# Performance work log

Hardware: AMD Instinct MI355X
Metric: run time of the kernel (lower is better)

Reference implementation:

```python
import jax, jax.numpy as jnp
import numpy as np

N, F_IN, H, C, D, NH, L, FF = 4096, 256, 2, 64, 128, 4, 2, 2048
DEG = 32


def setup_inputs() -> dict:
    key = jax.random.key(0)
    ks = jax.random.split(key, 32)
    s = 0.05
    # graph: random edges + self loops (PyG GATConv adds self loops)
    src = jax.random.randint(ks[0], (N * DEG,), 0, N)
    dst = jax.random.randint(ks[1], (N * DEG,), 0, N)
    loop = jnp.arange(N)
    edge_index = jnp.stack([jnp.concatenate([src, loop]),
                            jnp.concatenate([dst, loop])]).astype(jnp.int64)
    inp = {
        'x': jax.random.normal(ks[2], (N, F_IN), jnp.float32),
        'edge_index': edge_index,
        'enc_w1': jax.random.normal(ks[3], (F_IN, 128), jnp.float32) * s,
        'enc_b1': jnp.zeros((128,), jnp.float32),
        'enc_w2': jax.random.normal(ks[4], (128, D), jnp.float32) * s,
        'enc_b2': jnp.zeros((D,), jnp.float32),
        'gat_w': jax.random.normal(ks[5], (D, H * C), jnp.float32) * s,
        'gat_asrc': jax.random.normal(ks[6], (H, C), jnp.float32) * s,
        'gat_adst': jax.random.normal(ks[7], (H, C), jnp.float32) * s,
        'gat_bias': jnp.zeros((H * C,), jnp.float32),
        't_wq': jax.random.normal(ks[8], (L, D, D), jnp.float32) * s,
        't_bq': jnp.zeros((L, D), jnp.float32),
        't_wk': jax.random.normal(ks[9], (L, D, D), jnp.float32) * s,
        't_bk': jnp.zeros((L, D), jnp.float32),
        't_wv': jax.random.normal(ks[10], (L, D, D), jnp.float32) * s,
        't_bv': jnp.zeros((L, D), jnp.float32),
        't_wo': jax.random.normal(ks[11], (L, D, D), jnp.float32) * s,
        't_bo': jnp.zeros((L, D), jnp.float32),
        't_ln1_g': jnp.ones((L, D), jnp.float32),
        't_ln1_b': jnp.zeros((L, D), jnp.float32),
        't_ln2_g': jnp.ones((L, D), jnp.float32),
        't_ln2_b': jnp.zeros((L, D), jnp.float32),
        't_w1': jax.random.normal(ks[12], (L, D, FF), jnp.float32) * s,
        't_b1': jnp.zeros((L, FF), jnp.float32),
        't_w2': jax.random.normal(ks[13], (L, FF, D), jnp.float32) * s,
        't_b2': jnp.zeros((L, D), jnp.float32),
    }
    return inp


def _layer_norm(v, g, b):
    m = v.mean(-1, keepdims=True)
    var = v.var(-1, keepdims=True)
    return (v - m) / jnp.sqrt(var + 1e-5) * g + b


def _forward(x, edge_index, enc_w1, enc_b1, enc_w2, enc_b2,
             gat_w, gat_asrc, gat_adst, gat_bias,
             t_wq, t_bq, t_wk, t_bk, t_wv, t_bv, t_wo, t_bo,
             t_ln1_g, t_ln1_b, t_ln2_g, t_ln2_b, t_w1, t_b1, t_w2, t_b2):
    n = x.shape[0]
    # encoder MLP: Linear -> ReLU -> Linear
    h = jnp.maximum(x @ enc_w1 + enc_b1, 0.0) @ enc_w2 + enc_b2  # [N, D]
    # GATConv (concat heads), dropout inactive (eval)
    heads, ch = gat_asrc.shape
    hh = (h @ gat_w).reshape(n, heads, ch)                       # [N, H, C]
    src, dst = edge_index[0], edge_index[1]
    a_src = (hh * gat_asrc).sum(-1)                              # [N, H]
    a_dst = (hh * gat_adst).sum(-1)
    e = jax.nn.leaky_relu(a_src[src] + a_dst[dst], 0.2)          # [E, H]
    # segment softmax over destination nodes
    e_max = jax.ops.segment_max(e, dst, num_segments=n)
    e_exp = jnp.exp(e - e_max[dst])
    denom = jax.ops.segment_sum(e_exp, dst, num_segments=n)
    alpha = e_exp / denom[dst]                                   # [E, H]
    agg = jax.ops.segment_sum(alpha[:, :, None] * hh[src], dst, num_segments=n)
    y = agg.reshape(n, heads * ch) + gat_bias                    # [N, D]
    # TransformerEncoder (post-LN, relu FFN), unbatched sequence of N nodes
    d = y.shape[-1]
    dh = d // NH
    for l in range(t_wq.shape[0]):
        q = (y @ t_wq[l] + t_bq[l]).reshape(n, NH, dh)
        k = (y @ t_wk[l] + t_bk[l]).reshape(n, NH, dh)
        v = (y @ t_wv[l] + t_bv[l]).reshape(n, NH, dh)
        scores = jnp.einsum('nhd,mhd->hnm', q, k) / jnp.sqrt(jnp.float32(dh))
        p = jax.nn.softmax(scores, axis=-1)
        a = jnp.einsum('hnm,mhd->nhd', p, v).reshape(n, d)
        a = a @ t_wo[l] + t_bo[l]
        y = _layer_norm(y + a, t_ln1_g[l], t_ln1_b[l])
        f = jnp.maximum(y @ t_w1[l] + t_b1[l], 0.0) @ t_w2[l] + t_b2[l]
        y = _layer_norm(y + f, t_ln2_g[l], t_ln2_b[l])
    return y


def reference(x, edge_index, enc_w1, enc_b1, enc_w2, enc_b2,
              gat_w, gat_asrc, gat_adst, gat_bias,
              t_wq, t_bq, t_wk, t_bk, t_wv, t_bv, t_wo, t_bo,
              t_ln1_g, t_ln1_b, t_ln2_g, t_ln2_b, t_w1, t_b1, t_w2, t_b2):
    return _forward(x, edge_index, enc_w1, enc_b1, enc_w2, enc_b2,
                    gat_w, gat_asrc, gat_adst, gat_bias,
                    t_wq, t_bq, t_wk, t_bk, t_wv, t_bv, t_wo, t_bo,
                    t_ln1_g, t_ln1_b, t_ln2_g, t_ln2_b, t_w1, t_b1, t_w2, t_b2)
```

## Files before the change

### kernel.cpp

```cpp
#include <hip/hip_runtime.h>

typedef unsigned short u16;
typedef unsigned int u32;
typedef __attribute__((ext_vector_type(8))) short bh8;
typedef __attribute__((ext_vector_type(4))) float fx4;
typedef __attribute__((ext_vector_type(4))) short s4;
typedef __attribute__((ext_vector_type(2))) unsigned int u32x2;

#define QS 0.2550437194342803f

__device__ __forceinline__ u16 f2bf(float f) {
    unsigned u = __float_as_uint(f);
    u += 0x7fffu + ((u >> 16) & 1u);
    return (u16)(u >> 16);
}

__device__ __forceinline__ u32 cvtpk(float lo, float hi) {
    u32 r;
    asm("v_cvt_pk_bf16_f32 %0, %1, %2" : "=v"(r) : "v"(lo), "v"(hi));
    return r;
}

__global__ __launch_bounds__(256) void prep_kernel(
    const float* x, const float* ew1, const float* ew2, const float* gw,
    const float* wq, const float* wk, const float* wv, const float* wo,
    const float* w1, const float* w2,
    const float* bq, const float* bk, const float* bv,
    u16* xb, u16* ew1t, u16* ew2t, u16* gwt,
    u16* wqkvt, float* bqkv, u16* wot, u16* w1t, u16* w2t)
{
    __shared__ u16 tile[64 * 65];
    int bid = blockIdx.x;
    const int t = threadIdx.x;

    if (bid < 128) {
        const float4* x4 = (const float4*)x;
        s4* o4 = (s4*)xb;
        #pragma unroll
        for (int i = 0; i < 8; i++) {
            int fi = bid * 2048 + i * 256 + t;
            float4 v = x4[fi];
            s4 o = { (short)f2bf(v.x), (short)f2bf(v.y), (short)f2bf(v.z), (short)f2bf(v.w) };
            o4[fi] = o;
        }
        return;
    }
    bid -= 128;
    if (bid < 1) {
        for (int idx = t; idx < 768; idx += 256) {
            int l = idx / 384, n = idx % 384;
            float v;
            if (n < 128)      v = bq[l * 128 + n] * QS;
            else if (n < 256) v = bk[l * 128 + n - 128];
            else              v = bv[l * 128 + n - 256];
            bqkv[idx] = v;
        }
        return;
    }
    bid -= 1;

    const float* src; u16* dst; int R, C, tr, tc; float sc = 1.f;
    if (bid < 8)            { src = ew1; dst = ew1t; R = 256; C = 128; tr = bid >> 1; tc = bid & 1; }
    else if ((bid -= 8) < 4)  { src = ew2; dst = ew2t; R = 128; C = 128; tr = bid >> 1; tc = bid & 1; }
    else if ((bid -= 4) < 4)  { src = gw;  dst = gwt;  R = 128; C = 128; tr = bid >> 1; tc = bid & 1; }
    else if ((bid -= 4) < 24) {
        int l = bid / 12, r2 = bid % 12, which = r2 >> 2, i = r2 & 3;
        R = 128; C = 128; tr = i >> 1; tc = i & 1;
        if (which == 0)      { src = wq + l * 16384; dst = wqkvt + l * 49152;         sc = QS; }
        else if (which == 1) { src = wk + l * 16384; dst = wqkvt + l * 49152 + 16384; }
        else                 { src = wv + l * 16384; dst = wqkvt + l * 49152 + 32768; }
    }
    else if ((bid -= 24) < 8)   { int l = bid >> 2, i = bid & 3;  src = wo + l * 16384; dst = wot + l * 16384; R = 128; C = 128; tr = i >> 1; tc = i & 1; }
    else if ((bid -= 8) < 128)  { int l = bid >> 6, i = bid & 63; src = w1 + (size_t)l * 262144; dst = w1t + (size_t)l * 262144; R = 128;  C = 2048; tr = i & 1;  tc = i >> 1; }
    else { bid -= 128;            int l = bid >> 6, i = bid & 63; src = w2 + (size_t)l * 262144; dst = w2t + (size_t)l * 262144; R = 2048; C = 128;  tr = i >> 1; tc = i & 1; }

    const int r = t >> 2, cs = (t & 3) * 16;
    const float* sp = src + (size_t)(tr * 64 + r) * C + tc * 64 + cs;
    #pragma unroll
    for (int j = 0; j < 16; j++) tile[r * 65 + cs + j] = f2bf(sp[j] * sc);
    __syncthreads();
    u16* dp = dst + (size_t)(tc * 64 + r) * R + tr * 64 + cs;
    #pragma unroll
    for (int j = 0; j < 16; j++) dp[j] = tile[(cs + j) * 65 + r];
}

__global__ __launch_bounds__(256) void gemm_bf16(
    const u16* __restrict__ A, const u16* __restrict__ Bt,
    const float* __restrict__ bias,
    float* __restrict__ Cf, u16* __restrict__ Cb, float* __restrict__ Cpart,
    u16* __restrict__ Cvt,
    int M, int N, int K, int relu, int kchunk, int ldc)
{
    __shared__ __align__(16) u16 As[2][64][40];
    __shared__ __align__(16) u16 Bs[2][64][40];
    const int m0 = blockIdx.x * 64, n0 = blockIdx.y * 64, z = blockIdx.z;
    const int tid = threadIdx.x;
    const int lane = tid & 63, w = tid >> 6;
    const int wm = (w >> 1) * 32, wn = (w & 1) * 32;
    const int l15 = lane & 15, l4 = lane >> 4;
    const int srow = tid >> 2, skq = (tid & 3) * 8;
    const int k0 = z * kchunk;

    const u16* Ap = A + (size_t)(m0 + srow) * K + k0 + skq;
    const u16* Bp = Bt + (size_t)(n0 + srow) * K + k0 + skq;

    fx4 acc00 = {0,0,0,0}, acc01 = {0,0,0,0}, acc10 = {0,0,0,0}, acc11 = {0,0,0,0};

    *(int4*)&As[0][srow][skq] = *(const int4*)Ap;
    *(int4*)&Bs[0][srow][skq] = *(const int4*)Bp;

    const int niter = kchunk >> 5;
    for (int it = 0; it < niter; it++) {
        const int cur = it & 1;
        int4 ar, br;
        __syncthreads();
        if (it + 1 < niter) {
            ar = *(const int4*)(Ap + (it + 1) * 32);
            br = *(const int4*)(Bp + (it + 1) * 32);
        }
        bh8 a0 = *(const bh8*)&As[cur][wm + l15][l4 * 8];
        bh8 a1 = *(const bh8*)&As[cur][wm + 16 + l15][l4 * 8];
        bh8 b0 = *(const bh8*)&Bs[cur][wn + l15][l4 * 8];
        bh8 b1 = *(const bh8*)&Bs[cur][wn + 16 + l15][l4 * 8];
        acc00 = __builtin_amdgcn_mfma_f32_16x16x32_bf16(a0, b0, acc00, 0, 0, 0);
        acc01 = __builtin_amdgcn_mfma_f32_16x16x32_bf16(a0, b1, acc01, 0, 0, 0);
        acc10 = __builtin_amdgcn_mfma_f32_16x16x32_bf16(a1, b0, acc10, 0, 0, 0);
        acc11 = __builtin_amdgcn_mfma_f32_16x16x32_bf16(a1, b1, acc11, 0, 0, 0);
        if (it + 1 < niter) {
            *(int4*)&As[cur ^ 1][srow][skq] = ar;
            *(int4*)&Bs[cur ^ 1][srow][skq] = br;
        }
    }

    fx4* accs[2][2] = {{&acc00, &acc01}, {&acc10, &acc11}};
    #pragma unroll
    for (int i = 0; i < 2; i++)
        #pragma unroll
        for (int j = 0; j < 2; j++) {
            int colg = n0 + wn + j * 16 + l15;
            int rowb = m0 + wm + i * 16 + l4 * 4;
            if (Cpart) {
                float* cp = Cpart + (size_t)z * M * N;
                #pragma unroll
                for (int r = 0; r < 4; r++)
                    cp[(size_t)(rowb + r) * N + colg] = (*accs[i][j])[r];
                continue;
            }
            float bvv = bias ? bias[colg] : 0.f;
            float vals[4];
            #pragma unroll
            for (int r = 0; r < 4; r++) {
                float v = (*accs[i][j])[r] + bvv;
                vals[r] = relu ? fmaxf(v, 0.f) : v;
            }
            if (Cvt && colg >= 256) {
                s4 pk = { (short)f2bf(vals[0]), (short)f2bf(vals[1]),
                          (short)f2bf(vals[2]), (short)f2bf(vals[3]) };
                *(s4*)&Cvt[(size_t)(colg - 256) * 4096 + rowb] = pk;
            } else {
                #pragma unroll
                for (int r = 0; r < 4; r++) {
                    if (Cf) Cf[(size_t)(rowb + r) * ldc + colg] = vals[r];
                    if (Cb) Cb[(size_t)(rowb + r) * ldc + colg] = f2bf(vals[r]);
                }
            }
        }
}

__global__ __launch_bounds__(256) void enc2_gat(
    const u16* __restrict__ h1b, const u16* __restrict__ ew2t,
    const float* __restrict__ eb2, const u16* __restrict__ gwt,
    const float* __restrict__ gasrc, const float* __restrict__ gadst,
    float* __restrict__ hh, float* __restrict__ ansrc,
    float* __restrict__ andst, int* __restrict__ counts)
{
    __shared__ __align__(16) u16 As[32][136];
    __shared__ __align__(16) u16 Bs[2][128][40];
    __shared__ __align__(16) u16 Hb[32][136];
    __shared__ float Ct[32][132];
    const int m0 = blockIdx.x * 32;
    const int tid = threadIdx.x;
    const int lane = tid & 63, w = tid >> 6;
    const int wm = (w >> 1) * 16, wn = (w & 1) * 64;
    const int l15 = lane & 15, l4 = lane >> 4;

    if (tid < 32) counts[blockIdx.x * 32 + tid] = 0;

    {
        const int row = tid >> 3, c0 = (tid & 7) * 16;
        const u16* ap = h1b + (size_t)(m0 + row) * 128 + c0;
        *(int4*)&As[row][c0]     = *(const int4*)ap;
        *(int4*)&As[row][c0 + 8] = *(const int4*)(ap + 8);
    }
    {
        #pragma unroll
        for (int i = 0; i < 2; i++) {
            int s = tid + i * 256, r = s >> 2, c = (s & 3) * 8;
            *(int4*)&Bs[0][r][c] = *(const int4*)&ew2t[(size_t)r * 128 + c];
        }
    }

    fx4 acc[4] = {};
    for (int it = 0; it < 4; it++) {
        const int cur = it & 1;
        int4 br[2];
        __syncthreads();
        if (it < 3) {
            #pragma unroll
            for (int i = 0; i < 2; i++) {
                int s = tid + i * 256, r = s >> 2, c = (s & 3) * 8;
                br[i] = *(const int4*)&ew2t[(size_t)r * 128 + (it + 1) * 32 + c];
            }
        }
        bh8 af = *(const bh8*)&As[wm + l15][it * 32 + l4 * 8];
        #pragma unroll
        for (int nj = 0; nj < 4; nj++) {
            bh8 bf = *(const bh8*)&Bs[cur][wn + nj * 16 + l15][l4 * 8];
            acc[nj] = __builtin_amdgcn_mfma_f32_16x16x32_bf16(af, bf, acc[nj], 0, 0, 0);
        }
        if (it < 3) {
            #pragma unroll
            for (int i = 0; i < 2; i++) {
                int s = tid + i * 256, r = s >> 2, c = (s & 3) * 8;
                *(int4*)&Bs[cur ^ 1][r][c] = br[i];
            }
        }
    }

    #pragma unroll
    for (int nj = 0; nj < 4; nj++) {
        int cl = wn + nj * 16 + l15;
        float bvv = eb2[cl];
        #pragma unroll
        for (int r = 0; r < 4; r++)
            Hb[wm + l4 * 4 + r][cl] = f2bf(acc[nj][r] + bvv);
    }
    {
        #pragma unroll
        for (int i = 0; i < 2; i++) {
            int s = tid + i * 256, r = s >> 2, c = (s & 3) * 8;
            *(int4*)&Bs[0][r][c] = *(const int4*)&gwt[(size_t)r * 128 + c];
        }
    }

    fx4 acc2[4] = {};
    for (int it = 0; it < 4; it++) {
        const int cur = it & 1;
        int4 br[2];
        __syncthreads();
        if (it < 3) {
            #pragma unroll
            for (int i = 0; i < 2; i++) {
                int s = tid + i * 256, r = s >> 2, c = (s & 3) * 8;
                br[i] = *(const int4*)&gwt[(size_t)r * 128 + (it + 1) * 32 + c];
            }
        }
        bh8 af = *(const bh8*)&Hb[wm + l15][it * 32 + l4 * 8];
        #pragma unroll
        for (int nj = 0; nj < 4; nj++) {
            bh8 bf = *(const bh8*)&Bs[cur][wn + nj * 16 + l15][l4 * 8];
            acc2[nj] = __builtin_amdgcn_mfma_f32_16x16x32_bf16(af, bf, acc2[nj], 0, 0, 0);
        }
        if (it < 3) {
            #pragma unroll
            for (int i = 0; i < 2; i++) {
                int s = tid + i * 256, r = s >> 2, c = (s & 3) * 8;
                *(int4*)&Bs[cur ^ 1][r][c] = br[i];
            }
        }
    }

    #pragma unroll
    for (int nj = 0; nj < 4; nj++) {
        int cl = wn + nj * 16 + l15;
        #pragma unroll
        for (int r = 0; r < 4; r++) {
            int rl = wm + l4 * 4 + r;
            float v = acc2[nj][r];
            hh[(size_t)(m0 + rl) * 128 + cl] = v;
            Ct[rl][cl] = v;
        }
    }
    __syncthreads();

    const int row = tid >> 3, c0 = (tid & 7) * 16, head = c0 >> 6;
    float ps = 0.f, pd = 0.f;
    #pragma unroll
    for (int j = 0; j < 16; j++) {
        float v = Ct[row][c0 + j];
        int cc = (c0 + j) & 63;
        ps += v * gasrc[head * 64 + cc];
        pd += v * gadst[head * 64 + cc];
    }
    ps += __shfl_xor(ps, 1); pd += __shfl_xor(pd, 1);
    ps += __shfl_xor(ps, 2); pd += __shfl_xor(pd, 2);
    if ((tid & 3) == 0) {
        ansrc[(m0 + row) * 2 + head] = ps;
        andst[(m0 + row) * 2 + head] = pd;
    }
}

__global__ __launch_bounds__(256) void ffn_fused(
    const u16* __restrict__ A, const u16* __restrict__ W1t,
    const float* __restrict__ b1, const u16* __restrict__ W2t,
    float* __restrict__ part)
{
    __shared__ __align__(16) u16 Ab[64][136];
    __shared__ __align__(16) u16 Wb[64][136];
    __shared__ __align__(16) u16 Sb[64][72];
    const int m0 = blockIdx.x * 64, z = blockIdx.y;
    const int tid = threadIdx.x;
    const int lane = tid & 63, w = tid >> 6;
    const int wm = (w >> 1) * 32;
    const int wn = (w & 1) * 32;
    const int wn2 = (w & 1) * 64;
    const int l15 = lane & 15, l4 = lane >> 4;
    const int sr = tid >> 2, sc = (tid & 3) * 32;

    {
        const u16* ap = A + (size_t)(m0 + sr) * 128 + sc;
        #pragma unroll
        for (int i = 0; i < 4; i++)
            *(int4*)&Ab[sr][sc + i * 8] = *(const int4*)(ap + i * 8);
    }

    fx4 acc2[2][4] = {};

    for (int chunk = 0; chunk < 4; chunk++) {
        const int ffbase = z * 256 + chunk * 64;
        __syncthreads();
        {
            const u16* wp = W1t + (size_t)(ffbase + sr) * 128 + sc;
            #pragma unroll
            for (int i = 0; i < 4; i++)
                *(int4*)&Wb[sr][sc + i * 8] = *(const int4*)(wp + i * 8);
        }
        __syncthreads();

        fx4 s[2][2] = {};
        #pragma unroll
        for (int ks = 0; ks < 4; ks++) {
            bh8 af0 = *(const bh8*)&Ab[wm + l15][ks * 32 + l4 * 8];
            bh8 af1 = *(const bh8*)&Ab[wm + 16 + l15][ks * 32 + l4 * 8];
            bh8 bf0 = *(const bh8*)&Wb[wn + l15][ks * 32 + l4 * 8];
            bh8 bf1 = *(const bh8*)&Wb[wn + 16 + l15][ks * 32 + l4 * 8];
            s[0][0] = __builtin_amdgcn_mfma_f32_16x16x32_bf16(af0, bf0, s[0][0], 0, 0, 0);
            s[0][1] = __builtin_amdgcn_mfma_f32_16x16x32_bf16(af0, bf1, s[0][1], 0, 0, 0);
            s[1][0] = __builtin_amdgcn_mfma_f32_16x16x32_bf16(af1, bf0, s[1][0], 0, 0, 0);
            s[1][1] = __builtin_amdgcn_mfma_f32_16x16x32_bf16(af1, bf1, s[1][1], 0, 0, 0);
        }
        #pragma unroll
        for (int mi = 0; mi < 2; mi++)
            #pragma unroll
            for (int nj = 0; nj < 2; nj++) {
                float bv = b1[ffbase + wn + nj * 16 + l15];
                #pragma unroll
                for (int r = 0; r < 4; r++) {
                    float v = fmaxf(s[mi][nj][r] + bv, 0.f);
                    Sb[wm + mi * 16 + l4 * 4 + r][wn + nj * 16 + l15] = f2bf(v);
                }
            }
        __syncthreads();

        #pragma unroll
        for (int ks = 0; ks < 2; ks++) {
            bh8 af0 = *(const bh8*)&Sb[wm + l15][ks * 32 + l4 * 8];
            bh8 af1 = *(const bh8*)&Sb[wm + 16 + l15][ks * 32 + l4 * 8];
            #pragma unroll
            for (int nj = 0; nj < 4; nj++) {
                bh8 bf = *(const bh8*)&W2t[(size_t)(wn2 + nj * 16 + l15) * 2048 + ffbase + ks * 32 + l4 * 8];
                acc2[0][nj] = __builtin_amdgcn_mfma_f32_16x16x32_bf16(af0, bf, acc2[0][nj], 0, 0, 0);
                acc2[1][nj] = __builtin_amdgcn_mfma_f32_16x16x32_bf16(af1, bf, acc2[1][nj], 0, 0, 0);
            }
        }
    }

    float* cp = part + (size_t)z * 524288;
    #pragma unroll
    for (int mi = 0; mi < 2; mi++)
        #pragma unroll
        for (int nj = 0; nj < 4; nj++) {
            int colg = wn2 + nj * 16 + l15;
            int rowb = m0 + wm + mi * 16 + l4 * 4;
            #pragma unroll
            for (int r = 0; r < 4; r++)
                cp[(size_t)(rowb + r) * 128 + colg] = acc2[mi][nj][r];
        }
}

__global__ void count_edges(const int* __restrict__ dst, int* counts, int E) {
    int i = blockIdx.x * 256 + threadIdx.x;
    if (i < E) atomicAdd(&counts[dst[i]], 1);
}

__global__ __launch_bounds__(1024) void scan_kernel(const int* __restrict__ counts,
                                                    int* row_start, int* cursor) {
    __shared__ int wsum[16];
    int tid = threadIdx.x, lane = tid & 63, wv = tid >> 6;
    int b = tid * 4;
    int c0 = counts[b], c1 = counts[b+1], c2 = counts[b+2], c3 = counts[b+3];
    int sum = c0 + c1 + c2 + c3;
    int inc = sum;
    #pragma unroll
    for (int off = 1; off < 64; off <<= 1) {
        int v = __shfl_up(inc, off);
        if (lane >= off) inc += v;
    }
    if (lane == 63) wsum[wv] = inc;
    __syncthreads();
    int base = 0;
    #pragma unroll
    for (int i = 0; i < 16; i++) {
        int v = wsum[i];
        base += (i < wv) ? v : 0;
    }
    int excl = base + inc - sum;
    int r0 = excl, r1 = excl + c0, r2 = r1 + c1, r3 = r2 + c2;
    row_start[b] = r0; row_start[b+1] = r1; row_start[b+2] = r2; row_start[b+3] = r3;
    cursor[b] = r0; cursor[b+1] = r1; cursor[b+2] = r2; cursor[b+3] = r3;
    if (tid == 1023) row_start[4096] = base + inc;
}

__global__ void scatter_edges(const int* __restrict__ src, const int* __restrict__ dst,
                              int* cursor, int* csr_src, int E) {
    int i = blockIdx.x * 256 + threadIdx.x;
    if (i < E) { int pos = atomicAdd(&cursor[dst[i]], 1); csr_src[pos] = src[i]; }
}

__global__ __launch_bounds__(256) void gat_aggregate(
    const int* __restrict__ row_start, const int* __restrict__ csr_src,
    const float* __restrict__ an_src, const float* __restrict__ an_dst,
    const float* __restrict__ hh, const float* __restrict__ gbias,
    float* __restrict__ y32, u16* __restrict__ yb)
{
    int n = blockIdx.x, tid = threadIdx.x;
    const int lane = tid & 63, wv = tid >> 6;
    int start = row_start[n], end = row_start[n + 1];
    float ad0 = an_dst[n * 2 + 0], ad1 = an_dst[n * 2 + 1];
    __shared__ float rmx[4][2], rsm[4][2];
    __shared__ float sal0[128], sal1[128], sagg[256];
    __shared__ int sidx[128];

    float mx0 = -1e30f, mx1 = -1e30f;
    for (int i = start + tid; i < end; i += 256) {
        int s = csr_src[i];
        float e0 = an_src[s * 2 + 0] + ad0; e0 = e0 > 0.f ? e0 : 0.2f * e0;
        float e1 = an_src[s * 2 + 1] + ad1; e1 = e1 > 0.f ? e1 : 0.2f * e1;
        mx0 = fmaxf(mx0, e0); mx1 = fmaxf(mx1, e1);
    }
    for (int off = 32; off; off >>= 1) { mx0 = fmaxf(mx0, __shfl_down(mx0, off)); mx1 = fmaxf(mx1, __shfl_down(mx1, off)); }
    if (lane == 0) { rmx[wv][0] = mx0; rmx[wv][1] = mx1; }
    __syncthreads();
    mx0 = fmaxf(fmaxf(rmx[0][0], rmx[1][0]), fmaxf(rmx[2][0], rmx[3][0]));
    mx1 = fmaxf(fmaxf(rmx[0][1], rmx[1][1]), fmaxf(rmx[2][1], rmx[3][1]));

    float den0 = 0.f, den1 = 0.f;
    for (int i = start + tid; i < end; i += 256) {
        int s = csr_src[i];
        float e0 = an_src[s * 2 + 0] + ad0; e0 = e0 > 0.f ? e0 : 0.2f * e0;
        float e1 = an_src[s * 2 + 1] + ad1; e1 = e1 > 0.f ? e1 : 0.2f * e1;
        den0 += __expf(e0 - mx0); den1 += __expf(e1 - mx1);
    }
    for (int off = 32; off; off >>= 1) { den0 += __shfl_down(den0, off); den1 += __shfl_down(den1, off); }
    if (lane == 0) { rsm[wv][0] = den0; rsm[wv][1] = den1; }
    __syncthreads();
    den0 = rsm[0][0] + rsm[1][0] + rsm[2][0] + rsm[3][0];
    den1 = rsm[0][1] + rsm[1][1] + rsm[2][1] + rsm[3][1];
    float rd0 = 1.f / den0, rd1 = 1.f / den1;

    const int grp = tid >> 7, ch = tid & 127, head = ch >> 6;
    float agg = 0.f;
    for (int c0 = start; c0 < end; c0 += 128) {
        int cnt = min(128, end - c0);
        __syncthreads();
        if (tid < cnt) {
            int s = csr_src[c0 + tid];
            float e0 = an_src[s * 2 + 0] + ad0; e0 = e0 > 0.f ? e0 : 0.2f * e0;
            float e1 = an_src[s * 2 + 1] + ad1; e1 = e1 > 0.f ? e1 : 0.2f * e1;
            sal0[tid] = __expf(e0 - mx0) * rd0;
            sal1[tid] = __expf(e1 - mx1) * rd1;
            sidx[tid] = s;
        }
        __syncthreads();
        const float* sal = head ? sal1 : sal0;
        for (int j = grp; j < cnt; j += 2)
            agg += sal[j] * hh[(size_t)sidx[j] * 128 + ch];
    }
    sagg[tid] = agg;
    __syncthreads();
    if (tid < 128) {
        float v = sagg[tid] + sagg[tid + 128] + gbias[tid];
        y32[(size_t)n * 128 + tid] = v;
        yb[(size_t)n * 128 + tid] = f2bf(v);
    }
}

__global__ __launch_bounds__(256) void flash_attn_part(
    const u16* __restrict__ q, const u16* __restrict__ k,
    const u16* __restrict__ vt, float* __restrict__ po,
    float* __restrict__ pm, float* __restrict__ pl)
{
    __shared__ __align__(16) u16 Kb[2][64][40];
    __shared__ __align__(16) u16 Vb[2][32][72];
    __shared__ __align__(16) u16 Ps[4][16][72];
    const int q0 = blockIdx.x * 64, h = blockIdx.y, ch = blockIdx.z;
    const int tid = threadIdx.x;
    const int w = tid >> 6, lane = tid & 63, l15 = lane & 15, l4 = lane >> 4;

    bh8 qf = *(const bh8*)&q[(size_t)(q0 + w * 16 + l15) * 256 + h * 32 + l4 * 8];

    const int skey = tid >> 2, sds = (tid & 3) * 8;
    const int svd = tid >> 3, svk = (tid & 7) * 8;
    const u16* kgp = &k[(size_t)(ch * 1024 + skey) * 256 + h * 32 + sds];
    const u16* vgp = &vt[(size_t)(h * 32 + svd) * 4096 + ch * 1024 + svk];

    fx4 o0 = {0,0,0,0}, o1 = {0,0,0,0};
    float M = -1e30f, L = 0.f;

    *(int4*)&Kb[0][skey][sds] = *(const int4*)kgp;
    *(int4*)&Vb[0][svd][svk] = *(const int4*)vgp;

    for (int ti = 0; ti < 16; ti++) {
        const int cur = ti & 1;
        int4 kr, vr;
        __syncthreads();
        if (ti < 15) {
            kr = *(const int4*)(kgp + (size_t)(ti + 1) * 64 * 256);
            vr = *(const int4*)(vgp + (ti + 1) * 64);
        }

        fx4 s[4];
        #pragma unroll
        for (int sub = 0; sub < 4; sub++) {
            bh8 kf = *(const bh8*)&Kb[cur][sub * 16 + l15][l4 * 8];
            fx4 z = {0,0,0,0};
            s[sub] = __builtin_amdgcn_mfma_f32_16x16x32_bf16(kf, qf, z, 0, 0, 0);
        }
        float t0 = fmaxf(fmaxf(s[0][0], s[0][1]), s[0][2]);
        float t1 = fmaxf(fmaxf(s[0][3], s[1][0]), s[1][1]);
        float t2 = fmaxf(fmaxf(s[1][2], s[1][3]), s[2][0]);
        float t3 = fmaxf(fmaxf(s[2][1], s[2][2]), s[2][3]);
        float t4 = fmaxf(fmaxf(s[3][0], s[3][1]), s[3][2]);
        float pmax = fmaxf(fmaxf(fmaxf(t0, t1), t2), fmaxf(fmaxf(t3, t4), s[3][3]));
        pmax = fmaxf(pmax, __shfl_xor(pmax, 16));
        pmax = fmaxf(pmax, __shfl_xor(pmax, 32));
        if (!__all(pmax - M <= 8.0f)) {
            float f = __builtin_amdgcn_exp2f(M - pmax);
            M = pmax;
            o0 *= f; o1 *= f; L *= f;
        }

        #pragma unroll
        for (int sub = 0; sub < 4; sub++)
            #pragma unroll
            for (int r = 0; r < 4; r++)
                s[sub][r] = __builtin_amdgcn_exp2f(s[sub][r] - M);
        float ss0 = (s[0][0] + s[0][1]) + (s[0][2] + s[0][3]);
        float ss1 = (s[1][0] + s[1][1]) + (s[1][2] + s[1][3]);
        float ss2 = (s[2][0] + s[2][1]) + (s[2][2] + s[2][3]);
        float ss3 = (s[3][0] + s[3][1]) + (s[3][2] + s[3][3]);
        float lsum = (ss0 + ss1) + (ss2 + ss3);
        lsum += __shfl_xor(lsum, 16);
        lsum += __shfl_xor(lsum, 32);
        L += lsum;

        #pragma unroll
        for (int sub = 0; sub < 4; sub++) {
            u32x2 pk = { cvtpk(s[sub][0], s[sub][1]), cvtpk(s[sub][2], s[sub][3]) };
            *(u32x2*)&Ps[w][l15][sub * 16 + l4 * 4] = pk;
        }

        #pragma unroll
        for (int kc = 0; kc < 2; kc++) {
            bh8 bf  = *(const bh8*)&Ps[w][l15][kc * 32 + l4 * 8];
            bh8 af0 = *(const bh8*)&Vb[cur][l15][kc * 32 + l4 * 8];
            bh8 af1 = *(const bh8*)&Vb[cur][16 + l15][kc * 32 + l4 * 8];
            o0 = __builtin_amdgcn_mfma_f32_16x16x32_bf16(af0, bf, o0, 0, 0, 0);
            o1 = __builtin_amdgcn_mfma_f32_16x16x32_bf16(af1, bf, o1, 0, 0, 0);
        }

        if (ti < 15) {
            *(int4*)&Kb[cur ^ 1][skey][sds] = kr;
            *(int4*)&Vb[cur ^ 1][svd][svk] = vr;
        }
    }
    const int base = (blockIdx.x * 4 + h) * 4 + ch;
    const int qrow = w * 16 + l15;
    *(fx4*)&po[(size_t)(base * 64 + qrow) * 32 + l4 * 4]      = o0;
    *(fx4*)&po[(size_t)(base * 64 + qrow) * 32 + 16 + l4 * 4] = o1;
    if (l4 == 0) { pm[base * 64 + qrow] = M; pl[base * 64 + qrow] = L; }
}

__global__ __launch_bounds__(256) void oproj_cln(
    const float* __restrict__ po, const float* __restrict__ pm,
    const float* __restrict__ pl, const u16* __restrict__ Bt,
    const float* __restrict__ bias, const float* __restrict__ g,
    const float* __restrict__ b,
    float* __restrict__ y32, u16* __restrict__ yb)
{
    __shared__ __align__(16) u16 Ab[32][136];
    __shared__ __align__(16) u16 Bs[2][128][40];
    __shared__ float Ct[32][132];
    const int m0 = blockIdx.x * 32;
    const int tid = threadIdx.x;
    const int lane = tid & 63, w = tid >> 6;
    const int wm = (w >> 1) * 16, wn = (w & 1) * 64;
    const int l15 = lane & 15, l4 = lane >> 4;

    {
        const int row = tid >> 3, c0 = (tid & 7) * 16;
        const int gr = m0 + row, qb = gr >> 6, r64 = gr & 63, h = c0 >> 5;
        const int rb = (qb * 4 + h) * 4;
        float mv0 = pm[(rb + 0) * 64 + r64], mv1 = pm[(rb + 1) * 64 + r64];
        float mv2 = pm[(rb + 2) * 64 + r64], mv3 = pm[(rb + 3) * 64 + r64];
        float ms = fmaxf(fmaxf(mv0, mv1), fmaxf(mv2, mv3));
        float wc[4];
        wc[0] = __builtin_amdgcn_exp2f(mv0 - ms);
        wc[1] = __builtin_amdgcn_exp2f(mv1 - ms);
        wc[2] = __builtin_amdgcn_exp2f(mv2 - ms);
        wc[3] = __builtin_amdgcn_exp2f(mv3 - ms);
        float lsum = wc[0] * pl[(rb + 0) * 64 + r64] + wc[1] * pl[(rb + 1) * 64 + r64]
                   + wc[2] * pl[(rb + 2) * 64 + r64] + wc[3] * pl[(rb + 3) * 64 + r64];
        float rl = 1.f / lsum;
        const int cb = c0 & 31;
        float o[16] = {};
        #pragma unroll
        for (int c = 0; c < 4; c++) {
            const float* pp = po + ((size_t)((rb + c) * 64 + r64)) * 32 + cb;
            #pragma unroll
            for (int jj = 0; jj < 4; jj++) {
                fx4 v = *(const fx4*)(pp + jj * 4);
                o[jj * 4 + 0] += wc[c] * v[0];
                o[jj * 4 + 1] += wc[c] * v[1];
                o[jj * 4 + 2] += wc[c] * v[2];
                o[jj * 4 + 3] += wc[c] * v[3];
            }
        }
        #pragma unroll
        for (int j = 0; j < 16; j++)
            Ab[row][c0 + j] = f2bf(o[j] * rl);
    }

    {
        const int brow = tid >> 2, bkq = (tid & 3) * 8;
        *(int4*)&Bs[0][brow][bkq]      = *(const int4*)&Bt[(size_t)brow * 128 + bkq];
        *(int4*)&Bs[0][brow + 64][bkq] = *(const int4*)&Bt[(size_t)(brow + 64) * 128 + bkq];
    }

    fx4 acc[4] = {};
    const int brow = tid >> 2, bkq = (tid & 3) * 8;
    for (int it = 0; it < 4; it++) {
        const int cur = it & 1;
        int4 br0, br1;
        __syncthreads();
        if (it < 3) {
            br0 = *(const int4*)&Bt[(size_t)brow * 128 + (it + 1) * 32 + bkq];
            br1 = *(const int4*)&Bt[(size_t)(brow + 64) * 128 + (it + 1) * 32 + bkq];
        }
        bh8 af = *(const bh8*)&Ab[wm + l15][it * 32 + l4 * 8];
        #pragma unroll
        for (int nj = 0; nj < 4; nj++) {
            bh8 bf = *(const bh8*)&Bs[cur][wn + nj * 16 + l15][l4 * 8];
            acc[nj] = __builtin_amdgcn_mfma_f32_16x16x32_bf16(af, bf, acc[nj], 0, 0, 0);
        }
        if (it < 3) {
            *(int4*)&Bs[cur ^ 1][brow][bkq]      = br0;
            *(int4*)&Bs[cur ^ 1][brow + 64][bkq] = br1;
        }
    }

    #pragma unroll
    for (int nj = 0; nj < 4; nj++) {
        int cl = wn + nj * 16 + l15;
        float bvv = bias[cl];
        #pragma unroll
        for (int r = 0; r < 4; r++) {
            int rl = wm + l4 * 4 + r;
            Ct[rl][cl] = acc[nj][r] + bvv + y32[(size_t)(m0 + rl) * 128 + cl];
        }
    }
    __syncthreads();

    const int row = tid >> 3, c0 = (tid & 7) * 16;
    float s1 = 0.f, s2 = 0.f;
    #pragma unroll
    for (int j = 0; j < 16; j++) { float v = Ct[row][c0 + j]; s1 += v; s2 += v * v; }
    #pragma unroll
    for (int off = 1; off < 8; off <<= 1) { s1 += __shfl_xor(s1, off); s2 += __shfl_xor(s2, off); }
    float mean = s1 * (1.f / 128.f);
    float var = s2 * (1.f / 128.f) - mean * mean;
    float rstd = rsqrtf(var + 1e-5f);
    #pragma unroll
    for (int j = 0; j < 16; j++) {
        int col = c0 + j;
        float o = (Ct[row][col] - mean) * rstd * g[col] + b[col];
        y32[(size_t)(m0 + row) * 128 + col] = o;
        yb[(size_t)(m0 + row) * 128 + col] = f2bf(o);
    }
}

__global__ __launch_bounds__(128) void add_ln_p(
    const float* __restrict__ y, const float* __restrict__ part, int nz,
    const float* __restrict__ bias,
    const float* __restrict__ g, const float* __restrict__ b,
    float* __restrict__ out32, u16* __restrict__ outb)
{
    int n = blockIdx.x, tid = threadIdx.x;
    float v = y[(size_t)n * 128 + tid] + bias[tid];
    for (int z = 0; z < nz; z++) v += part[(size_t)z * 524288 + n * 128 + tid];
    float sacc = v;
    for (int off = 32; off; off >>= 1) sacc += __shfl_down(sacc, off);
    __shared__ float sm[2], sv[2];
    if ((tid & 63) == 0) sm[tid >> 6] = sacc;
    __syncthreads();
    float mean = (sm[0] + sm[1]) * (1.f / 128.f);
    float d = v - mean;
    float qacc = d * d;
    for (int off = 32; off; off >>= 1) qacc += __shfl_down(qacc, off);
    if ((tid & 63) == 0) sv[tid >> 6] = qacc;
    __syncthreads();
    float var = (sv[0] + sv[1]) * (1.f / 128.f);
    float o = d * rsqrtf(var + 1e-5f) * g[tid] + b[tid];
    out32[(size_t)n * 128 + tid] = o;
    outb[(size_t)n * 128 + tid] = f2bf(o);
}

extern "C" void kernel_launch(void* const* d_in, const int* in_sizes, int n_in,
                              void* d_out, int out_size, void* d_ws, size_t ws_size,
                              hipStream_t stream)
{
    const float* x     = (const float*)d_in[0];
    const int*   ei    = (const int*)  d_in[1];
    const float* ew1   = (const float*)d_in[2];
    const float* eb1   = (const float*)d_in[3];
    const float* ew2   = (const float*)d_in[4];
    const float* eb2   = (const float*)d_in[5];
    const float* gw    = (const float*)d_in[6];
    const float* gasrc = (const float*)d_in[7];
    const float* gadst = (const float*)d_in[8];
    const float* gbias = (const float*)d_in[9];
    const float* wq    = (const float*)d_in[10];
    const float* bq    = (const float*)d_in[11];
    const float* wk    = (const float*)d_in[12];
    const float* bk    = (const float*)d_in[13];
    const float* wv    = (const float*)d_in[14];
    const float* bv    = (const float*)d_in[15];
    const float* wo    = (const float*)d_in[16];
    const float* bo    = (const float*)d_in[17];
    const float* ln1g  = (const float*)d_in[18];
    const float* ln1b  = (const float*)d_in[19];
    const float* ln2g  = (const float*)d_in[20];
    const float* ln2b  = (const float*)d_in[21];
    const float* w1    = (const float*)d_in[22];
    const float* b1    = (const float*)d_in[23];
    const float* w2    = (const float*)d_in[24];
    const float* b2    = (const float*)d_in[25];

    const int E = in_sizes[1] / 2;
    const int* esrc = ei;
    const int* edst = ei + E;

    char* p = (char*)d_ws;
    auto alloc = [&](size_t bytes) -> void* {
        void* r = (void*)p;
        p += (bytes + 255) & ~(size_t)255;
        return r;
    };
    u16* xb    = (u16*)alloc(4096 * 256 * 2);
    u16* ew1t  = (u16*)alloc(128 * 256 * 2);
    u16* ew2t  = (u16*)alloc(128 * 128 * 2);
    u16* gwt   = (u16*)alloc(128 * 128 * 2);
    u16* wqkvt = (u16*)alloc(2 * 384 * 128 * 2);
    float* bqkv = (float*)alloc(2 * 384 * 4);
    u16* wot   = (u16*)alloc(2 * 128 * 128 * 2);
    u16* w1t   = (u16*)alloc(2 * 2048 * 128 * 2);
    u16* w2t   = (u16*)alloc(2 * 128 * 2048 * 2);
    u16* h1b   = (u16*)alloc(4096 * 128 * 2);
    float* hh  = (float*)alloc(4096 * 128 * 4);
    float* ansrc = (float*)alloc(4096 * 2 * 4);
    float* andst = (float*)alloc(4096 * 2 * 4);
    int* counts    = (int*)alloc(4096 * 4);
    int* row_start = (int*)alloc(4097 * 4);
    int* cursor    = (int*)alloc(4096 * 4);
    int* csr_src   = (int*)alloc((size_t)E * 4);
    float* y32 = (float*)alloc(4096 * 128 * 4);
    u16* yb    = (u16*)alloc(4096 * 128 * 2);
    u16* qkvb  = (u16*)alloc((size_t)4096 * 256 * 2);
    u16* vtb   = (u16*)alloc(4096 * 128 * 2);
    float* po  = (float*)alloc((size_t)64 * 4 * 4 * 64 * 32 * 4);
    float* pm  = (float*)alloc(64 * 4 * 4 * 64 * 4);
    float* pl  = (float*)alloc(64 * 4 * 4 * 64 * 4);
    float* ffpart = (float*)alloc((size_t)8 * 4096 * 128 * 4);

    prep_kernel<<<433, 256, 0, stream>>>(x, ew1, ew2, gw, wq, wk, wv, wo, w1, w2,
                                         bq, bk, bv,
                                         xb, ew1t, ew2t, gwt, wqkvt, bqkv, wot, w1t, w2t);

    gemm_bf16<<<dim3(64, 2), 256, 0, stream>>>(xb, ew1t, eb1, nullptr, h1b, nullptr, nullptr, 4096, 128, 256, 1, 256, 128);
    enc2_gat<<<128, 256, 0, stream>>>(h1b, ew2t, eb2, gwt, gasrc, gadst, hh, ansrc, andst, counts);
    count_edges<<<(E + 255) / 256, 256, 0, stream>>>(edst, counts, E);
    scan_kernel<<<1, 1024, 0, stream>>>(counts, row_start, cursor);
    scatter_edges<<<(E + 255) / 256, 256, 0, stream>>>(esrc, edst, cursor, csr_src, E);
    gat_aggregate<<<4096, 256, 0, stream>>>(row_start, csr_src, ansrc, andst, hh, gbias, y32, yb);

    for (int l = 0; l < 2; l++) {
        gemm_bf16<<<dim3(64, 6), 256, 0, stream>>>(yb, wqkvt + l * 49152, bqkv + l * 384, nullptr, qkvb, nullptr, vtb, 4096, 384, 128, 0, 128, 256);
        flash_attn_part<<<dim3(64, 4, 4), 256, 0, stream>>>(qkvb, qkvb + 128, vtb, po, pm, pl);
        oproj_cln<<<128, 256, 0, stream>>>(po, pm, pl, wot + l * 16384, bo + l * 128, ln1g + l * 128, ln1b + l * 128, y32, yb);
        ffn_fused<<<dim3(64, 8), 256, 0, stream>>>(yb, w1t + (size_t)l * 262144, b1 + l * 2048, w2t + (size_t)l * 262144, ffpart);
        float* outp = (l == 1) ? (float*)d_out : y32;
        add_ln_p<<<4096, 128, 0, stream>>>(y32, ffpart, 8, b2 + l * 128, ln2g + l * 128, ln2b + l * 128, outp, yb);
    }
}
```

Baseline: 184.0 us.

## Fuse first encoder GEMM into encoder/GAT kernel and halve FFN split-K partials

Folds the first encoder layer (x @ W1 + b1, ReLU) into the encoder/GAT projection kernel. This drops a separate GEMM launch and the h1b round trip through global memory, and the freed LDS A buffer is reused for the second intermediate. It also changes the FFN split from 8 to 4 partitions of the hidden dimension, so each block loops over 512 hidden units. That means fewer partial sums to write and reduce in add_ln_p, but the grid is half as large, which lowers parallelism.

```diff
diff --git a/kernel.cpp b/kernel.cpp
--- a/kernel.cpp
+++ b/kernel.cpp
@@ -167,14 +167,16 @@
         }
 }
 
-__global__ __launch_bounds__(256) void enc2_gat(
-    const u16* __restrict__ h1b, const u16* __restrict__ ew2t,
-    const float* __restrict__ eb2, const u16* __restrict__ gwt,
+__global__ __launch_bounds__(256) void encoder_gat(
+    const u16* __restrict__ xb, const u16* __restrict__ ew1t,
+    const float* __restrict__ eb1,
+    const u16* __restrict__ ew2t, const float* __restrict__ eb2,
+    const u16* __restrict__ gwt,
     const float* __restrict__ gasrc, const float* __restrict__ gadst,
     float* __restrict__ hh, float* __restrict__ ansrc,
     float* __restrict__ andst, int* __restrict__ counts)
 {
-    __shared__ __align__(16) u16 As[32][136];
+    __shared__ __align__(16) u16 As[32][264];
     __shared__ __align__(16) u16 Bs[2][128][40];
     __shared__ __align__(16) u16 Hb[32][136];
     __shared__ float Ct[32][132];
@@ -187,59 +189,59 @@
     if (tid < 32) counts[blockIdx.x * 32 + tid] = 0;
 
     {
-        const int row = tid >> 3, c0 = (tid & 7) * 16;
-        const u16* ap = h1b + (size_t)(m0 + row) * 128 + c0;
-        *(int4*)&As[row][c0]     = *(const int4*)ap;
-        *(int4*)&As[row][c0 + 8] = *(const int4*)(ap + 8);
+        const int row = tid >> 3, c0 = (tid & 7) * 32;
+        const u16* ap = xb + (size_t)(m0 + row) * 256 + c0;
+        #pragma unroll
+        for (int i = 0; i < 4; i++)
+            *(int4*)&As[row][c0 + i * 8] = *(const int4*)(ap + i * 8);
+    }
+    {
+        #pragma unroll
+        for (int i = 0; i < 2; i++) {
+            int s = tid + i * 256, r = s >> 2, c = (s & 3) * 8;
+            *(int4*)&Bs[0][r][c] = *(const int4*)&ew1t[(size_t)r * 256 + c];
+        }
+    }
+
+    fx4 acc[4] = {};
+    for (int it = 0; it < 8; it++) {
+        const int cur = it & 1;
+        int4 br[2];
+        __syncthreads();
+        if (it < 7) {
+            #pragma unroll
+            for (int i = 0; i < 2; i++) {
+                int s = tid + i * 256, r = s >> 2, c = (s & 3) * 8;
+                br[i] = *(const int4*)&ew1t[(size_t)r * 256 + (it + 1) * 32 + c];
+            }
+        }
+        bh8 af = *(const bh8*)&As[wm + l15][it * 32 + l4 * 8];
+        #pragma unroll
+        for (int nj = 0; nj < 4; nj++) {
+            bh8 bf = *(const bh8*)&Bs[cur][wn + nj * 16 + l15][l4 * 8];
+            acc[nj] = __builtin_amdgcn_mfma_f32_16x16x32_bf16(af, bf, acc[nj], 0, 0, 0);
+        }
+        if (it < 7) {
+            #pragma unroll
+            for (int i = 0; i < 2; i++) {
+                int s = tid + i * 256, r = s >> 2, c = (s & 3) * 8;
+                *(int4*)&Bs[cur ^ 1][r][c] = br[i];
+            }
+        }
+    }
+    #pragma unroll
+    for (int nj = 0; nj < 4; nj++) {
+        int cl = wn + nj * 16 + l15;
+        float bvv = eb1[cl];
+        #pragma unroll
+        for (int r = 0; r < 4; r++)
+            Hb[wm + l4 * 4 + r][cl] = f2bf(fmaxf(acc[nj][r] + bvv, 0.f));
     }
     {
         #pragma unroll
         for (int i = 0; i < 2; i++) {
             int s = tid + i * 256, r = s >> 2, c = (s & 3) * 8;
             *(int4*)&Bs[0][r][c] = *(const int4*)&ew2t[(size_t)r * 128 + c];
-        }
-    }
-
-    fx4 acc[4] = {};
-    for (int it = 0; it < 4; it++) {
-        const int cur = it & 1;
-        int4 br[2];
-        __syncthreads();
-        if (it < 3) {
-            #pragma unroll
-            for (int i = 0; i < 2; i++) {
-                int s = tid + i * 256, r = s >> 2, c = (s & 3) * 8;
-                br[i] = *(const int4*)&ew2t[(size_t)r * 128 + (it + 1) * 32 + c];
-            }
-        }
-        bh8 af = *(const bh8*)&As[wm + l15][it * 32 + l4 * 8];
-        #pragma unroll
-        for (int nj = 0; nj < 4; nj++) {
-            bh8 bf = *(const bh8*)&Bs[cur][wn + nj * 16 + l15][l4 * 8];
-            acc[nj] = __builtin_amdgcn_mfma_f32_16x16x32_bf16(af, bf, acc[nj], 0, 0, 0);
-        }
-        if (it < 3) {
-            #pragma unroll
-            for (int i = 0; i < 2; i++) {
-                int s = tid + i * 256, r = s >> 2, c = (s & 3) * 8;
-                *(int4*)&Bs[cur ^ 1][r][c] = br[i];
-            }
-        }
-    }
-
-    #pragma unroll
-    for (int nj = 0; nj < 4; nj++) {
-        int cl = wn + nj * 16 + l15;
-        float bvv = eb2[cl];
-        #pragma unroll
-        for (int r = 0; r < 4; r++)
-            Hb[wm + l4 * 4 + r][cl] = f2bf(acc[nj][r] + bvv);
-    }
-    {
-        #pragma unroll
-        for (int i = 0; i < 2; i++) {
-            int s = tid + i * 256, r = s >> 2, c = (s & 3) * 8;
-            *(int4*)&Bs[0][r][c] = *(const int4*)&gwt[(size_t)r * 128 + c];
         }
     }
 
@@ -252,7 +254,7 @@
             #pragma unroll
             for (int i = 0; i < 2; i++) {
                 int s = tid + i * 256, r = s >> 2, c = (s & 3) * 8;
-                br[i] = *(const int4*)&gwt[(size_t)r * 128 + (it + 1) * 32 + c];
+                br[i] = *(const int4*)&ew2t[(size_t)r * 128 + (it + 1) * 32 + c];
             }
         }
         bh8 af = *(const bh8*)&Hb[wm + l15][it * 32 + l4 * 8];
@@ -269,14 +271,57 @@
             }
         }
     }
-
+    u16 (*Hb2)[136] = (u16(*)[136])&As[0][0];
     #pragma unroll
     for (int nj = 0; nj < 4; nj++) {
         int cl = wn + nj * 16 + l15;
+        float bvv = eb2[cl];
+        #pragma unroll
+        for (int r = 0; r < 4; r++)
+            Hb2[wm + l4 * 4 + r][cl] = f2bf(acc2[nj][r] + bvv);
+    }
+    {
+        #pragma unroll
+        for (int i = 0; i < 2; i++) {
+            int s = tid + i * 256, r = s >> 2, c = (s & 3) * 8;
+            *(int4*)&Bs[0][r][c] = *(const int4*)&gwt[(size_t)r * 128 + c];
+        }
+    }
+
+    fx4 acc3[4] = {};
+    for (int it = 0; it < 4; it++) {
+        const int cur = it & 1;
+        int4 br[2];
+        __syncthreads();
+        if (it < 3) {
+            #pragma unroll
+            for (int i = 0; i < 2; i++) {
+                int s = tid + i * 256, r = s >> 2, c = (s & 3) * 8;
+                br[i] = *(const int4*)&gwt[(size_t)r * 128 + (it + 1) * 32 + c];
+            }
+        }
+        bh8 af = *(const bh8*)&Hb2[wm + l15][it * 32 + l4 * 8];
+        #pragma unroll
+        for (int nj = 0; nj < 4; nj++) {
+            bh8 bf = *(const bh8*)&Bs[cur][wn + nj * 16 + l15][l4 * 8];
+            acc3[nj] = __builtin_amdgcn_mfma_f32_16x16x32_bf16(af, bf, acc3[nj], 0, 0, 0);
+        }
+        if (it < 3) {
+            #pragma unroll
+            for (int i = 0; i < 2; i++) {
+                int s = tid + i * 256, r = s >> 2, c = (s & 3) * 8;
+                *(int4*)&Bs[cur ^ 1][r][c] = br[i];
+            }
+        }
+    }
+
+    #pragma unroll
+    for (int nj = 0; nj < 4; nj++) {
+        int cl = wn + nj * 16 + l15;
         #pragma unroll
         for (int r = 0; r < 4; r++) {
             int rl = wm + l4 * 4 + r;
-            float v = acc2[nj][r];
+            float v = acc3[nj][r];
             hh[(size_t)(m0 + rl) * 128 + cl] = v;
             Ct[rl][cl] = v;
         }
@@ -326,8 +371,8 @@
 
     fx4 acc2[2][4] = {};
 
-    for (int chunk = 0; chunk < 4; chunk++) {
-        const int ffbase = z * 256 + chunk * 64;
+    for (int chunk = 0; chunk < 8; chunk++) {
+        const int ffbase = z * 512 + chunk * 64;
         __syncthreads();
         {
             const u16* wp = W1t + (size_t)(ffbase + sr) * 128 + sc;
@@ -775,7 +820,6 @@
     u16* wot   = (u16*)alloc(2 * 128 * 128 * 2);
     u16* w1t   = (u16*)alloc(2 * 2048 * 128 * 2);
     u16* w2t   = (u16*)alloc(2 * 128 * 2048 * 2);
-    u16* h1b   = (u16*)alloc(4096 * 128 * 2);
     float* hh  = (float*)alloc(4096 * 128 * 4);
     float* ansrc = (float*)alloc(4096 * 2 * 4);
     float* andst = (float*)alloc(4096 * 2 * 4);
@@ -790,14 +834,14 @@
     float* po  = (float*)alloc((size_t)64 * 4 * 4 * 64 * 32 * 4);
     float* pm  = (float*)alloc(64 * 4 * 4 * 64 * 4);
     float* pl  = (float*)alloc(64 * 4 * 4 * 64 * 4);
-    float* ffpart = (float*)alloc((size_t)8 * 4096 * 128 * 4);
+    float* ffpart = (float*)alloc((size_t)4 * 4096 * 128 * 4);
 
     prep_kernel<<<433, 256, 0, stream>>>(x, ew1, ew2, gw, wq, wk, wv, wo, w1, w2,
                                          bq, bk, bv,
                                          xb, ew1t, ew2t, gwt, wqkvt, bqkv, wot, w1t, w2t);
 
-    gemm_bf16<<<dim3(64, 2), 256, 0, stream>>>(xb, ew1t, eb1, nullptr, h1b, nullptr, nullptr, 4096, 128, 256, 1, 256, 128);
-    enc2_gat<<<128, 256, 0, stream>>>(h1b, ew2t, eb2, gwt, gasrc, gadst, hh, ansrc, andst, counts);
+    encoder_gat<<<128, 256, 0, stream>>>(xb, ew1t, eb1, ew2t, eb2, gwt,
+                                         gasrc, gadst, hh, ansrc, andst, counts);
     count_edges<<<(E + 255) / 256, 256, 0, stream>>>(edst, counts, E);
     scan_kernel<<<1, 1024, 0, stream>>>(counts, row_start, cursor);
     scatter_edges<<<(E + 255) / 256, 256, 0, stream>>>(esrc, edst, cursor, csr_src, E);
@@ -807,8 +851,8 @@
         gemm_bf16<<<dim3(64, 6), 256, 0, stream>>>(yb, wqkvt + l * 49152, bqkv + l * 384, nullptr, qkvb, nullptr, vtb, 4096, 384, 128, 0, 128, 256);
         flash_attn_part<<<dim3(64, 4, 4), 256, 0, stream>>>(qkvb, qkvb + 128, vtb, po, pm, pl);
         oproj_cln<<<128, 256, 0, stream>>>(po, pm, pl, wot + l * 16384, bo + l * 128, ln1g + l * 128, ln1b + l * 128, y32, yb);
-        ffn_fused<<<dim3(64, 8), 256, 0, stream>>>(yb, w1t + (size_t)l * 262144, b1 + l * 2048, w2t + (size_t)l * 262144, ffpart);
+        ffn_fused<<<dim3(64, 4), 256, 0, stream>>>(yb, w1t + (size_t)l * 262144, b1 + l * 2048, w2t + (size_t)l * 262144, ffpart);
         float* outp = (l == 1) ? (float*)d_out : y32;
-        add_ln_p<<<4096, 128, 0, stream>>>(y32, ffpart, 8, b2 + l * 128, ln2g + l * 128, ln2b + l * 128, outp, yb);
-    }
-}
+        add_ln_p<<<4096, 128, 0, stream>>>(y32, ffpart, 4, b2 + l * 128, ln2g + l * 128, ln2b + l * 128, outp, yb);
+    }
+}
```

Result: slower. 194.2 us (+5.5%).
